# Optimization experiments

Hardware: AMD Instinct MI355X
Metric: run time of the kernel (lower is better)

The kernel has to match this reference:

```python
import jax, jax.numpy as jnp
import numpy as np

jax.config.update("jax_enable_x64", True)

ALPHA = 10.0
N_LAMBDA = 1.0
NON_REG = False


def setup_inputs() -> dict:
    key = jax.random.key(0)
    k1, k2 = jax.random.split(key)
    x = jax.random.normal(k1, (2, 3, 8192), dtype=jnp.float32)
    gt = jax.random.normal(k2, (2, 3, 8192), dtype=jnp.float32)
    return {"x": x, "gt": gt}


def _chamfer_raw(x, y):
    # x: [B, D, N], y: [B, D, M]; torch version upcasts to double
    x = x.astype(jnp.float64)
    y = y.astype(jnp.float64)
    xx = jnp.sum(x * x, axis=1)                      # [B, N]
    yy = jnp.sum(y * y, axis=1)                      # [B, M]
    zz = jnp.einsum("bdn,bdm->bnm", x, y)           # [B, N, M]
    P = xx[:, :, None] + yy[:, None, :] - 2.0 * zz   # squared L2 dists
    dist1 = jnp.min(P, axis=2)                       # [B, N] closest y for each x
    idx1 = jnp.argmin(P, axis=2)
    dist2 = jnp.min(P, axis=1)                       # [B, M] closest x for each y
    idx2 = jnp.argmin(P, axis=1)
    return dist1, dist2, idx1, idx2


def reference(x, gt):
    x = x.astype(jnp.float32)
    gt = gt.astype(jnp.float32)
    B, _, n_x = x.shape
    _, _, n_gt = gt.shape
    if NON_REG:
        frac_12 = max(1.0, n_x / n_gt)
        frac_21 = max(1.0, n_gt / n_x)
    else:
        frac_12 = n_x / n_gt
        frac_21 = n_gt / n_x

    dist1, dist2, idx1, idx2 = _chamfer_raw(x, gt)
    exp_dist1 = jnp.exp(-dist1 * ALPHA)
    exp_dist2 = jnp.exp(-dist2 * ALPHA)

    brow = jnp.arange(B)[:, None]
    # count1[b, j] = #x-points whose NN is gt point j
    count1 = jnp.zeros((B, n_gt), jnp.int64).at[brow, idx1].add(1)
    weight1 = count1[brow, idx1].astype(exp_dist1.dtype) ** N_LAMBDA
    weight1 = (1.0 / (weight1 + 1e-06)) * frac_21
    loss1 = jnp.mean(1.0 - exp_dist1 * weight1, axis=1)

    count2 = jnp.zeros((B, n_x), jnp.int64).at[brow, idx2].add(1)
    weight2 = count2[brow, idx2].astype(exp_dist2.dtype) ** N_LAMBDA
    weight2 = (1.0 / (weight2 + 1e-06)) * frac_12
    loss2 = jnp.mean(1.0 - exp_dist2 * weight2, axis=1)

    loss = (loss1 + loss2) / 2.0
    return jnp.mean(loss)
```

## Files before the change

### kernel.cpp

```cpp
#include <hip/hip_runtime.h>

#define BATCH   2
#define NPT     8192
#define THREADS 256
#define PPT     8
#define OWN     (THREADS * PPT)
#define OPP     128
#define NCI     (NPT / OWN)
#define NCJ     (NPT / OPP)

typedef unsigned long long u64;

__global__ __launch_bounds__(THREADS) void dacd_pair_kernel(
    const float* __restrict__ x, const float* __restrict__ gt,
    u64* __restrict__ bestAll)
{
    __shared__ float4 sg[OPP];

    const int id  = blockIdx.x;
    const int dir = id & 1;
    const int b   = (id >> 1) & 1;
    const int ci  = (id >> 2) & (NCI - 1);
    const int cj  = id >> 4;

    const float* own = dir == 0 ? x : gt;
    const float* opp = dir == 0 ? gt : x;
    u64* best = bestAll + (size_t)dir * (BATCH * NPT) + (size_t)b * NPT;

    const int t = threadIdx.x;
    const float* ob = own + (size_t)b * (3 * NPT);
    const float* pb = opp + (size_t)b * (3 * NPT);

    if (t < OPP) {
        const int j = cj * OPP + t;
        const float gx = pb[j], gy = pb[NPT + j], gz = pb[2 * NPT + j];
        sg[t] = make_float4(-2.0f * gx, -2.0f * gy, -2.0f * gz,
                            fmaf(gx, gx, fmaf(gy, gy, gz * gz)));
    }

    float px[PPT], py[PPT], pz[PPT], bm[PPT];
    int   bj[PPT];
    const int i0 = ci * OWN + t;
    #pragma unroll
    for (int p = 0; p < PPT; ++p) {
        const int i = i0 + p * THREADS;
        px[p] = ob[i];
        py[p] = ob[NPT + i];
        pz[p] = ob[2 * NPT + i];
        bm[p] = INFINITY;
        bj[p] = 0;
    }
    __syncthreads();

    #pragma unroll 4
    for (int j = 0; j < OPP; ++j) {
        const float4 h = sg[j];
        #pragma unroll
        for (int p = 0; p < PPT; ++p) {
            const float m = fmaf(px[p], h.x, fmaf(py[p], h.y, fmaf(pz[p], h.z, h.w)));
            if (m < bm[p]) { bm[p] = m; bj[p] = j; }
        }
    }

    #pragma unroll
    for (int p = 0; p < PPT; ++p) {
        const float pp = fmaf(px[p], px[p], fmaf(py[p], py[p], pz[p] * pz[p]));
        const float d  = fmaxf(pp + bm[p], 0.0f);
        const u64 pk = ((u64)__float_as_uint(d) << 32) | (unsigned)(cj * OPP + bj[p]);
        atomicMax(&best[i0 + p * THREADS], ~pk);
    }
}

__global__ __launch_bounds__(256) void dacd_count_kernel(
    const u64* __restrict__ bestAll, int* __restrict__ countAll)
{
    const int i = blockIdx.x * 256 + threadIdx.x;
    const int b = i >> 13;
    const unsigned j1 = (unsigned)(~bestAll[i]);
    atomicAdd(&countAll[(b << 13) | j1], 1);
    const unsigned j2 = (unsigned)(~bestAll[BATCH * NPT + i]);
    atomicAdd(&countAll[BATCH * NPT + ((b << 13) | j2)], 1);
}

#define LGRID 64
__global__ __launch_bounds__(256) void dacd_loss_kernel(
    const u64* __restrict__ bestAll, const int* __restrict__ countAll,
    double* __restrict__ acc, unsigned* __restrict__ ticket,
    float* __restrict__ out)
{
    const int t = threadIdx.x;
    double local = 0.0;
    #pragma unroll
    for (int q = 0; q < 2; ++q) {
        const int k = (blockIdx.x * 512) + q * 256 + t;
        const u64 v = ~bestAll[k];
        const float d = __uint_as_float((unsigned)(v >> 32));
        const unsigned j = (unsigned)v;
        const int dirb = k >> 13;
        const int cnt = countAll[(dirb << 13) | j];
        const float w = 1.0f / ((float)cnt + 1e-6f);
        local += (double)(1.0f - expf(-10.0f * d) * w);
    }
    #pragma unroll
    for (int off = 32; off > 0; off >>= 1)
        local += __shfl_down(local, off, 64);
    __shared__ double red[4];
    const int lane = t & 63, wid = t >> 6;
    if (lane == 0) red[wid] = local;
    __syncthreads();
    if (t == 0) {
        atomicAdd(acc, red[0] + red[1] + red[2] + red[3]);
        __threadfence();
        const unsigned old = atomicAdd(ticket, 1u);
        if (old == LGRID - 1) {
            __threadfence();
            const double s = atomicAdd(acc, 0.0);
            out[0] = (float)(s * (1.0 / (2.0 * BATCH * NPT)));
        }
    }
}

extern "C" void kernel_launch(void* const* d_in, const int* in_sizes, int n_in,
                              void* d_out, int out_size, void* d_ws, size_t ws_size,
                              hipStream_t stream)
{
    const float* x  = (const float*)d_in[0];
    const float* gt = (const float*)d_in[1];
    float* out = (float*)d_out;

    u64* bestAll  = (u64*)d_ws;
    int* countAll = (int*)(bestAll + 2 * BATCH * NPT);
    double* acc   = (double*)(countAll + 2 * BATCH * NPT);
    unsigned* ticket = (unsigned*)(acc + 1);

    const size_t zeroBytes =
        (size_t)2 * BATCH * NPT * (sizeof(u64) + sizeof(int)) + sizeof(double) + 2 * sizeof(unsigned);
    hipMemsetAsync(bestAll, 0, zeroBytes, stream);

    dacd_pair_kernel<<<2 * BATCH * NCI * NCJ, THREADS, 0, stream>>>(x, gt, bestAll);
    dacd_count_kernel<<<(BATCH * NPT) / 256, 256, 0, stream>>>(bestAll, countAll);
    dacd_loss_kernel<<<LGRID, 256, 0, stream>>>(bestAll, countAll, acc, ticket, out);
}
```

Baseline: 93.72 us.

## Fuse pair, count and loss kernels into one persistent kernel with grid barriers

Merges the three kernels into one launch and uses atomic-counter grid barriers between the nearest-neighbour, histogram and loss phases. The workspace zeroing moves into the kernel, so the large memset shrinks to clearing only the three barrier counters. This removes two kernel launches, the inter-kernel gaps and most of the memset. It relies on all 1024 blocks being co-resident, which risks deadlock or serialization if occupancy cannot hold the full grid, and adds spin-wait and barrier overhead.

```diff
diff --git a/kernel.cpp b/kernel.cpp
--- a/kernel.cpp
+++ b/kernel.cpp
@@ -8,114 +8,142 @@
 #define OPP     128
 #define NCI     (NPT / OWN)
 #define NCJ     (NPT / OPP)
+#define GRID    (2 * BATCH * NCI * NCJ)
+#define TOTAL   (2 * BATCH * NPT)
 
 typedef unsigned long long u64;
 
-__global__ __launch_bounds__(THREADS) void dacd_pair_kernel(
+__device__ __forceinline__ void grid_sync(unsigned* bar) {
+    __syncthreads();
+    if (threadIdx.x == 0) {
+        __hip_atomic_fetch_add(bar, 1u, __ATOMIC_ACQ_REL, __HIP_MEMORY_SCOPE_AGENT);
+        while (__hip_atomic_load(bar, __ATOMIC_ACQUIRE, __HIP_MEMORY_SCOPE_AGENT) < GRID)
+            __builtin_amdgcn_s_sleep(2);
+    }
+    __syncthreads();
+}
+
+__global__ __launch_bounds__(THREADS) void dacd_fused_kernel(
     const float* __restrict__ x, const float* __restrict__ gt,
-    u64* __restrict__ bestAll)
+    u64* __restrict__ bestAll,
+    int* __restrict__ countAll,
+    double* __restrict__ acc, unsigned* __restrict__ ticket,
+    unsigned* __restrict__ bar,
+    float* __restrict__ out)
 {
     __shared__ float4 sg[OPP];
+    __shared__ double red[4];
 
-    const int id  = blockIdx.x;
-    const int dir = id & 1;
-    const int b   = (id >> 1) & 1;
-    const int ci  = (id >> 2) & (NCI - 1);
-    const int cj  = id >> 4;
+    const int t   = threadIdx.x;
+    const int tid = blockIdx.x * THREADS + t;
 
-    const float* own = dir == 0 ? x : gt;
-    const float* opp = dir == 0 ? gt : x;
-    u64* best = bestAll + (size_t)dir * (BATCH * NPT) + (size_t)b * NPT;
+    if (tid < TOTAL) {
+        __hip_atomic_store(&bestAll[tid], 0ull, __ATOMIC_RELAXED, __HIP_MEMORY_SCOPE_AGENT);
+        __hip_atomic_store(&countAll[tid], 0,   __ATOMIC_RELAXED, __HIP_MEMORY_SCOPE_AGENT);
+    }
+    if (tid == 0) {
+        __hip_atomic_store(acc, 0.0,  __ATOMIC_RELAXED, __HIP_MEMORY_SCOPE_AGENT);
+        __hip_atomic_store(ticket, 0u, __ATOMIC_RELAXED, __HIP_MEMORY_SCOPE_AGENT);
+    }
+    grid_sync(&bar[0]);
 
-    const int t = threadIdx.x;
-    const float* ob = own + (size_t)b * (3 * NPT);
-    const float* pb = opp + (size_t)b * (3 * NPT);
+    {
+        const int id  = blockIdx.x;
+        const int dir = id & 1;
+        const int b   = (id >> 1) & 1;
+        const int ci  = (id >> 2) & (NCI - 1);
+        const int cj  = id >> 4;
 
-    if (t < OPP) {
-        const int j = cj * OPP + t;
-        const float gx = pb[j], gy = pb[NPT + j], gz = pb[2 * NPT + j];
-        sg[t] = make_float4(-2.0f * gx, -2.0f * gy, -2.0f * gz,
-                            fmaf(gx, gx, fmaf(gy, gy, gz * gz)));
-    }
+        const float* own = dir == 0 ? x : gt;
+        const float* opp = dir == 0 ? gt : x;
+        u64* best = bestAll + (size_t)dir * (BATCH * NPT) + (size_t)b * NPT;
 
-    float px[PPT], py[PPT], pz[PPT], bm[PPT];
-    int   bj[PPT];
-    const int i0 = ci * OWN + t;
-    #pragma unroll
-    for (int p = 0; p < PPT; ++p) {
-        const int i = i0 + p * THREADS;
-        px[p] = ob[i];
-        py[p] = ob[NPT + i];
-        pz[p] = ob[2 * NPT + i];
-        bm[p] = INFINITY;
-        bj[p] = 0;
-    }
-    __syncthreads();
+        const float* ob = own + (size_t)b * (3 * NPT);
+        const float* pb = opp + (size_t)b * (3 * NPT);
 
-    #pragma unroll 4
-    for (int j = 0; j < OPP; ++j) {
-        const float4 h = sg[j];
+        if (t < OPP) {
+            const int j = cj * OPP + t;
+            const float gx = pb[j], gy = pb[NPT + j], gz = pb[2 * NPT + j];
+            sg[t] = make_float4(-2.0f * gx, -2.0f * gy, -2.0f * gz,
+                                fmaf(gx, gx, fmaf(gy, gy, gz * gz)));
+        }
+
+        float px[PPT], py[PPT], pz[PPT], bm[PPT];
+        int   bj[PPT];
+        const int i0 = ci * OWN + t;
         #pragma unroll
         for (int p = 0; p < PPT; ++p) {
-            const float m = fmaf(px[p], h.x, fmaf(py[p], h.y, fmaf(pz[p], h.z, h.w)));
-            if (m < bm[p]) { bm[p] = m; bj[p] = j; }
+            const int i = i0 + p * THREADS;
+            px[p] = ob[i];
+            py[p] = ob[NPT + i];
+            pz[p] = ob[2 * NPT + i];
+            bm[p] = INFINITY;
+            bj[p] = 0;
+        }
+        __syncthreads();
+
+        #pragma unroll 4
+        for (int j = 0; j < OPP; ++j) {
+            const float4 h = sg[j];
+            #pragma unroll
+            for (int p = 0; p < PPT; ++p) {
+                const float m = fmaf(px[p], h.x,
+                                fmaf(py[p], h.y,
+                                fmaf(pz[p], h.z, h.w)));
+                if (m < bm[p]) { bm[p] = m; bj[p] = j; }
+            }
+        }
+
+        #pragma unroll
+        for (int p = 0; p < PPT; ++p) {
+            const float pp = fmaf(px[p], px[p], fmaf(py[p], py[p], pz[p] * pz[p]));
+            const float d  = fmaxf(pp + bm[p], 0.0f);
+            const u64 pk = ((u64)__float_as_uint(d) << 32)
+                         | (unsigned)(cj * OPP + bj[p]);
+            atomicMax(&best[i0 + p * THREADS], ~pk);
         }
     }
+    grid_sync(&bar[1]);
 
-    #pragma unroll
-    for (int p = 0; p < PPT; ++p) {
-        const float pp = fmaf(px[p], px[p], fmaf(py[p], py[p], pz[p] * pz[p]));
-        const float d  = fmaxf(pp + bm[p], 0.0f);
-        const u64 pk = ((u64)__float_as_uint(d) << 32) | (unsigned)(cj * OPP + bj[p]);
-        atomicMax(&best[i0 + p * THREADS], ~pk);
+    if (tid < TOTAL) {
+        const u64 v = ~__hip_atomic_load(&bestAll[tid], __ATOMIC_RELAXED,
+                                         __HIP_MEMORY_SCOPE_AGENT);
+        const int dirb = tid >> 13;
+        atomicAdd(&countAll[(dirb << 13) | (unsigned)v], 1);
     }
-}
+    grid_sync(&bar[2]);
 
-__global__ __launch_bounds__(256) void dacd_count_kernel(
-    const u64* __restrict__ bestAll, int* __restrict__ countAll)
-{
-    const int i = blockIdx.x * 256 + threadIdx.x;
-    const int b = i >> 13;
-    const unsigned j1 = (unsigned)(~bestAll[i]);
-    atomicAdd(&countAll[(b << 13) | j1], 1);
-    const unsigned j2 = (unsigned)(~bestAll[BATCH * NPT + i]);
-    atomicAdd(&countAll[BATCH * NPT + ((b << 13) | j2)], 1);
-}
-
-#define LGRID 64
-__global__ __launch_bounds__(256) void dacd_loss_kernel(
-    const u64* __restrict__ bestAll, const int* __restrict__ countAll,
-    double* __restrict__ acc, unsigned* __restrict__ ticket,
-    float* __restrict__ out)
-{
-    const int t = threadIdx.x;
-    double local = 0.0;
-    #pragma unroll
-    for (int q = 0; q < 2; ++q) {
-        const int k = (blockIdx.x * 512) + q * 256 + t;
-        const u64 v = ~bestAll[k];
-        const float d = __uint_as_float((unsigned)(v >> 32));
-        const unsigned j = (unsigned)v;
-        const int dirb = k >> 13;
-        const int cnt = countAll[(dirb << 13) | j];
-        const float w = 1.0f / ((float)cnt + 1e-6f);
-        local += (double)(1.0f - expf(-10.0f * d) * w);
-    }
-    #pragma unroll
-    for (int off = 32; off > 0; off >>= 1)
-        local += __shfl_down(local, off, 64);
-    __shared__ double red[4];
-    const int lane = t & 63, wid = t >> 6;
-    if (lane == 0) red[wid] = local;
-    __syncthreads();
-    if (t == 0) {
-        atomicAdd(acc, red[0] + red[1] + red[2] + red[3]);
-        __threadfence();
-        const unsigned old = atomicAdd(ticket, 1u);
-        if (old == LGRID - 1) {
-            __threadfence();
-            const double s = atomicAdd(acc, 0.0);
-            out[0] = (float)(s * (1.0 / (2.0 * BATCH * NPT)));
+    {
+        double local = 0.0;
+        if (tid < TOTAL) {
+            const u64 v = ~__hip_atomic_load(&bestAll[tid], __ATOMIC_RELAXED,
+                                             __HIP_MEMORY_SCOPE_AGENT);
+            const float d = __uint_as_float((unsigned)(v >> 32));
+            const int dirb = tid >> 13;
+            const int cnt = __hip_atomic_load(
+                &countAll[(dirb << 13) | (unsigned)v],
+                __ATOMIC_RELAXED, __HIP_MEMORY_SCOPE_AGENT);
+            const float w = 1.0f / ((float)cnt + 1e-6f);
+            local = (double)(1.0f - expf(-10.0f * d) * w);
+        }
+        if (blockIdx.x < TOTAL / THREADS) {
+            #pragma unroll
+            for (int off = 32; off > 0; off >>= 1)
+                local += __shfl_down(local, off, 64);
+            const int lane = t & 63, wid = t >> 6;
+            if (lane == 0) red[wid] = local;
+            __syncthreads();
+            if (t == 0)
+                atomicAdd(acc, red[0] + red[1] + red[2] + red[3]);
+        }
+        if (t == 0) {
+            const unsigned old = __hip_atomic_fetch_add(
+                ticket, 1u, __ATOMIC_ACQ_REL, __HIP_MEMORY_SCOPE_AGENT);
+            if (old == GRID - 1) {
+                const double s = __hip_atomic_load(acc, __ATOMIC_RELAXED,
+                                                   __HIP_MEMORY_SCOPE_AGENT);
+                out[0] = (float)(s * (1.0 / (double)TOTAL));
+            }
         }
     }
 }
@@ -128,16 +156,14 @@
     const float* gt = (const float*)d_in[1];
     float* out = (float*)d_out;
 
-    u64* bestAll  = (u64*)d_ws;
-    int* countAll = (int*)(bestAll + 2 * BATCH * NPT);
-    double* acc   = (double*)(countAll + 2 * BATCH * NPT);
+    u64* bestAll     = (u64*)d_ws;
+    int* countAll    = (int*)(bestAll + TOTAL);
+    double* acc      = (double*)(countAll + TOTAL);
     unsigned* ticket = (unsigned*)(acc + 1);
+    unsigned* bar    = ticket + 1;
 
-    const size_t zeroBytes =
-        (size_t)2 * BATCH * NPT * (sizeof(u64) + sizeof(int)) + sizeof(double) + 2 * sizeof(unsigned);
-    hipMemsetAsync(bestAll, 0, zeroBytes, stream);
+    hipMemsetAsync(bar, 0, 3 * sizeof(unsigned), stream);
 
-    dacd_pair_kernel<<<2 * BATCH * NCI * NCJ, THREADS, 0, stream>>>(x, gt, bestAll);
-    dacd_count_kernel<<<(BATCH * NPT) / 256, 256, 0, stream>>>(bestAll, countAll);
-    dacd_loss_kernel<<<LGRID, 256, 0, stream>>>(bestAll, countAll, acc, ticket, out);
+    dacd_fused_kernel<<<GRID, THREADS, 0, stream>>>(
+        x, gt, bestAll, countAll, acc, ticket, bar, out);
 }
```

Measured after the change: 282.3 us. 3.01x slower.
